# Kernel optimization log

Hardware: AMD Instinct MI355X
Metric: run time of the kernel (lower is better)

The kernel has to match this reference:

```python
import jax, jax.numpy as jnp
import numpy as np

# dims: S spaces, B batch, T tokens, D = dense_dim = concept_dim, K codebook size
S, B, T, D, K = 8, 8, 2048, 64, 512
BN_EPS = 1e-3  # keras BatchNormalization default


def setup_inputs() -> dict:
    key = jax.random.key(0)
    k0, k1, k2 = jax.random.split(key, 3)
    x = jax.random.normal(k0, (B, T, D), jnp.float32)
    W = jax.random.normal(k1, (S, D, D), jnp.float32) * 0.1   # per-space Dense kernels
    b = jnp.zeros((S, D), jnp.float32)                         # per-space Dense biases
    gamma = jnp.ones((S, D), jnp.float32)                      # BN scale
    beta = jnp.zeros((S, D), jnp.float32)                      # BN shift
    bn_mean = jnp.zeros((S, D), jnp.float32)                   # BN moving mean
    bn_var = jnp.ones((S, D), jnp.float32)                     # BN moving var
    E = jax.random.normal(k2, (S, K, D), jnp.float32)          # per-space codebooks
    return dict(x=x, W=W, b=b, gamma=gamma, beta=beta,
                bn_mean=bn_mean, bn_var=bn_var, E=E)


def reference(x, W, b, gamma, beta, bn_mean, bn_var, E):
    # per-space projection: Dense -> BatchNorm (inference) -> softmax gate
    proj = jnp.einsum('btd,sde->sbte', x, W) + b[:, None, None, :]          # [S,B,T,D]
    inv = jax.lax.rsqrt(bn_var + BN_EPS)
    bn = gamma[:, None, None, :] * (proj - bn_mean[:, None, None, :]) * inv[:, None, None, :] \
         + beta[:, None, None, :]
    att = jax.nn.softmax(bn, axis=-1)
    z = x[None] * att                                                       # z_e_att, [S,B,T,D]

    # squared euclidean distance to each code; argmin(norm) == argmin(dist^2)
    d2 = (jnp.sum(z * z, axis=-1, keepdims=True)
          - 2.0 * jnp.einsum('sbtc,skc->sbtk', z, E)
          + jnp.sum(E * E, axis=-1)[:, None, None, :])                      # [S,B,T,K]
    z_k = jnp.argmin(d2, axis=-1)                                           # [S,B,T] int

    # gather nearest codes per space, then add_n over spaces (set_att != 0)
    z_q_s = E[jnp.arange(S)[:, None, None], z_k]                            # [S,B,T,D]
    z_q = jnp.sum(z_q_s, axis=0)                                            # [B,T,D]
    z_e = jnp.sum(z, axis=0)                                                # [B,T,D]
    z_k = z_k.astype(jnp.int64) if z_k.dtype != jnp.int64 else z_k          # tf.argmin -> int64
    return z_q, z_e, z_k
```

## Files before the change

### kernel.cpp

```cpp
#include <hip/hip_runtime.h>
#include <cfloat>
#include <cmath>

#define SN 8
#define DN 64
#define KN 512
#define NN 16384
#define CK 64
#define REPAIR_THR 2e-3f
#define MAXFLAG 65536

#define WS_CNT 0
#define WS_SCL 16
#define WS_OFF (16 + SN*DN)
#define WS_E2  (WS_OFF + SN*DN)
#define WS_ENT (WS_E2 + SN*KN)
#define WS_WTH (WS_ENT + MAXFLAG)
#define WS_WTL (WS_WTH + SN*64*32)
#define WS_EH  (WS_WTL + SN*64*32)
#define WS_EL  (WS_EH + SN*KN*32)
#define WS_ZP  (WS_EL + SN*KN*32)
#define WS_END (WS_ZP + SN*NN*DN)

#define LDS_XH   0
#define LDS_XL   8192
#define LDS_WE   16384
#define LDS_ZH   32768
#define LDS_ZL   40960
#define LDS_TAIL 49152
#define LDS_TOTAL 50176

#define FB_LDS_R2    17408
#define FB_LDS_TAIL  33792
#define FB_LDS_TOTAL 34816

typedef __attribute__((ext_vector_type(8))) short bf16x8;
typedef __attribute__((ext_vector_type(4))) short s16x4;
typedef __attribute__((ext_vector_type(4))) float f32x4;

__device__ inline short bf_hi(float f, float& rem) {
    unsigned u = __float_as_uint(f);
    unsigned r = (u + 0x7fffu + ((u >> 16) & 1u)) & 0xffff0000u;
    rem = f - __uint_as_float(r);
    return (short)(r >> 16);
}
__device__ inline short bf_rn(float f) {
    unsigned u = __float_as_uint(f);
    return (short)((u + 0x7fffu + ((u >> 16) & 1u)) >> 16);
}
__device__ inline void cvt4(float a, float b, float c, float d, s16x4& h, s16x4& l) {
    float r0, r1, r2, r3;
    h.x = bf_hi(a, r0); h.y = bf_hi(b, r1); h.z = bf_hi(c, r2); h.w = bf_hi(d, r3);
    l.x = bf_rn(r0); l.y = bf_rn(r1); l.z = bf_rn(r2); l.w = bf_rn(r3);
}
__device__ inline float bf2f(unsigned short h) {
    return __uint_as_float(((unsigned)h) << 16);
}

__global__ void prep_kernel(const float* __restrict__ b, const float* __restrict__ gamma,
                            const float* __restrict__ beta, const float* __restrict__ bmean,
                            const float* __restrict__ bvar, const float* __restrict__ E,
                            float* __restrict__ ws) {
    int tid = blockIdx.x * 256 + threadIdx.x;
    if (tid < SN * KN) {
        const float* er = E + (size_t)tid * DN;
        double a = 0.0;
        for (int d = 0; d < DN; ++d) { double v = (double)er[d]; a = fma(v, v, a); }
        ws[WS_E2 + tid] = (float)a;
    }
    int u = tid - SN * KN;
    if (u >= 0 && u < SN * DN) {
        double inv = 1.0 / sqrt((double)bvar[u] + 0.001);
        double sc  = (double)gamma[u] * inv;
        ws[WS_SCL + u] = (float)sc;
        ws[WS_OFF + u] = (float)(((double)b[u] - (double)bmean[u]) * sc + (double)beta[u]);
    }
}

__global__ void prep2_kernel(const float* __restrict__ E, float* __restrict__ ws) {
    int idx = blockIdx.x * 256 + threadIdx.x;
    int sk = idx >> 4, c4 = idx & 15;
    int k = sk & (KN - 1);
    float4 g = ((const float4*)E)[(size_t)sk * 16 + c4];
    s16x4 h4, l4;
    cvt4(g.x, g.y, g.z, g.w, h4, l4);
    size_t off = ((size_t)sk * 128 + c4 * 8) ^ ((k & 7) << 4);
    *(s16x4*)((char*)(ws + WS_EH) + off) = h4;
    *(s16x4*)((char*)(ws + WS_EL) + off) = l4;
}

__global__ void prep2w_kernel(const float* __restrict__ W, float* __restrict__ ws) {
    __shared__ float wt[64][65];
    int s = blockIdx.x;
    int tid = threadIdx.x;
    #pragma unroll
    for (int r = 0; r < 4; ++r) {
        int i = r * 256 + tid;
        float4 g = ((const float4*)W)[(size_t)s * 1024 + i];
        int d = i >> 4, c4 = i & 15;
        wt[d][c4 * 4 + 0] = g.x; wt[d][c4 * 4 + 1] = g.y;
        wt[d][c4 * 4 + 2] = g.z; wt[d][c4 * 4 + 3] = g.w;
    }
    __syncthreads();
    #pragma unroll
    for (int r = 0; r < 4; ++r) {
        int j = r * 256 + tid;
        int e = j >> 4, c4 = j & 15;
        s16x4 h4, l4;
        cvt4(wt[c4 * 4 + 0][e], wt[c4 * 4 + 1][e], wt[c4 * 4 + 2][e], wt[c4 * 4 + 3][e], h4, l4);
        size_t off = ((size_t)(s * 64 + e) * 128 + c4 * 8) ^ ((e & 7) << 4);
        *(s16x4*)((char*)(ws + WS_WTH) + off) = h4;
        *(s16x4*)((char*)(ws + WS_WTL) + off) = l4;
    }
}

__launch_bounds__(256, 3)
__global__ void main_kernel(const float* __restrict__ x, float* __restrict__ ws,
                            float* __restrict__ out, int entcap) {
    extern __shared__ char smraw[];
    float* tailf = (float*)(smraw + LDS_TAIL);
    float* e2s = tailf;
    float* scl = tailf + 64;
    float* ofl = tailf + 128;
    float* zzs = tailf + 192;

    const int tid = threadIdx.x;
    const int s  = blockIdx.y;
    const int n0 = blockIdx.x * 64;

    const int lane = tid & 63;
    const int w    = tid >> 6;
    const int cc   = lane & 15;
    const int kq   = lane >> 4;

    {
        const float4* xg4 = (const float4*)x;
        #pragma unroll
        for (int r = 0; r < 4; ++r) {
            int i = r * 256 + tid;
            float4 g = xg4[n0 * 16 + i];
            int row = i >> 4, c4 = i & 15;
            s16x4 h4, l4;
            cvt4(g.x, g.y, g.z, g.w, h4, l4);
            int off = (row * 128 + c4 * 8) ^ ((row & 7) << 4);
            *(s16x4*)(smraw + LDS_XH + off) = h4;
            *(s16x4*)(smraw + LDS_XL + off) = l4;
        }
        const float4* wth4 = (const float4*)((const char*)(ws + WS_WTH) + (size_t)s * 8192);
        const float4* wtl4 = (const float4*)((const char*)(ws + WS_WTL) + (size_t)s * 8192);
        #pragma unroll
        for (int r = 0; r < 2; ++r) {
            int i = r * 256 + tid;
            ((float4*)(smraw + LDS_WE))[i] = wth4[i];
            ((float4*)(smraw + LDS_WE + 8192))[i] = wtl4[i];
        }
        if (tid < 64) { scl[tid] = ws[WS_SCL + s * 64 + tid]; ofl[tid] = ws[WS_OFF + s * 64 + tid]; }
    }
    __syncthreads();

    const int arow  = w * 16 + cc;
    const int abase = arow * 128 + kq * 16;
    const int axor  = (arow & 7) << 4;

    f32x4 pa[4];
    #pragma unroll
    for (int nt = 0; nt < 4; ++nt) pa[nt] = (f32x4){0.f, 0.f, 0.f, 0.f};
    #pragma unroll
    for (int ks = 0; ks < 2; ++ks) {
        int aoff = (abase + ks * 64) ^ axor;
        bf16x8 ah = *(const bf16x8*)(smraw + LDS_XH + aoff);
        bf16x8 al = *(const bf16x8*)(smraw + LDS_XL + aoff);
        #pragma unroll
        for (int nt = 0; nt < 4; ++nt) {
            int brow = nt * 16 + cc;
            int boff = (brow * 128 + kq * 16 + ks * 64) ^ ((brow & 7) << 4);
            bf16x8 bh = *(const bf16x8*)(smraw + LDS_WE + boff);
            bf16x8 bl = *(const bf16x8*)(smraw + LDS_WE + 8192 + boff);
            pa[nt] = __builtin_amdgcn_mfma_f32_16x16x32_bf16(ah, bh, pa[nt], 0, 0, 0);
            pa[nt] = __builtin_amdgcn_mfma_f32_16x16x32_bf16(ah, bl, pa[nt], 0, 0, 0);
            pa[nt] = __builtin_amdgcn_mfma_f32_16x16x32_bf16(al, bh, pa[nt], 0, 0, 0);
        }
    }

    {
        float sclv[4], oflv[4];
        #pragma unroll
        for (int nt = 0; nt < 4; ++nt) { sclv[nt] = scl[nt * 16 + cc]; oflv[nt] = ofl[nt * 16 + cc]; }
        #pragma unroll
        for (int r = 0; r < 4; ++r) {
            int t = w * 16 + kq * 4 + r;
            float v0 = fmaf(pa[0][r], sclv[0], oflv[0]);
            float v1 = fmaf(pa[1][r], sclv[1], oflv[1]);
            float v2 = fmaf(pa[2][r], sclv[2], oflv[2]);
            float v3 = fmaf(pa[3][r], sclv[3], oflv[3]);
            float mx = fmaxf(fmaxf(v0, v1), fmaxf(v2, v3));
            mx = fmaxf(mx, __shfl_xor(mx, 1)); mx = fmaxf(mx, __shfl_xor(mx, 2));
            mx = fmaxf(mx, __shfl_xor(mx, 4)); mx = fmaxf(mx, __shfl_xor(mx, 8));
            float e0 = expf(v0 - mx), e1 = expf(v1 - mx), e2v = expf(v2 - mx), e3 = expf(v3 - mx);
            float sm = e0 + e1 + e2v + e3;
            sm += __shfl_xor(sm, 1); sm += __shfl_xor(sm, 2);
            sm += __shfl_xor(sm, 4); sm += __shfl_xor(sm, 8);
            float inv = 1.0f / sm;
            float att[4] = { e0 * inv, e1 * inv, e2v * inv, e3 * inv };
            float zz = 0.f;
            int txor = (t & 7) << 4;
            #pragma unroll
            for (int nt = 0; nt < 4; ++nt) {
                int e = nt * 16 + cc;
                int xoff = (t * 128 + e * 2) ^ txor;
                float xv = bf2f(*(const unsigned short*)(smraw + LDS_XH + xoff))
                         + bf2f(*(const unsigned short*)(smraw + LDS_XL + xoff));
                float z = xv * att[nt];
                zz += z * z;
                float rem; short zh = bf_hi(z, rem); short zl = bf_rn(rem);
                *(short*)(smraw + LDS_ZH + xoff) = zh;
                *(short*)(smraw + LDS_ZL + xoff) = zl;
                ws[WS_ZP + ((size_t)s * NN + n0 + t) * DN + e] = z;
            }
            zz += __shfl_xor(zz, 1); zz += __shfl_xor(zz, 2);
            zz += __shfl_xor(zz, 4); zz += __shfl_xor(zz, 8);
            if (cc == 0) zzs[t] = zz;
        }
    }
    __syncthreads();

    float zzv[4];
    #pragma unroll
    for (int r = 0; r < 4; ++r) zzv[r] = zzs[w * 16 + kq * 4 + r];

    float m1[4], m2[4]; int k1[4];
    #pragma unroll
    for (int r = 0; r < 4; ++r) { m1[r] = FLT_MAX; m2[r] = FLT_MAX; k1[r] = 0x7fffffff; }

    for (int kk = 0; kk < KN; kk += CK) {
        __syncthreads();
        {
            const float4* gh4 = (const float4*)((const char*)(ws + WS_EH) + (size_t)(s * KN + kk) * 128);
            const float4* gl4 = (const float4*)((const char*)(ws + WS_EL) + (size_t)(s * KN + kk) * 128);
            #pragma unroll
            for (int r = 0; r < 2; ++r) {
                int i = r * 256 + tid;
                ((float4*)(smraw + LDS_WE))[i] = gh4[i];
                ((float4*)(smraw + LDS_WE + 8192))[i] = gl4[i];
            }
        }
        if (tid < 64) e2s[tid] = ws[WS_E2 + s * KN + kk + tid];
        __syncthreads();

        f32x4 acc[4];
        #pragma unroll
        for (int nt = 0; nt < 4; ++nt) acc[nt] = (f32x4){0.f, 0.f, 0.f, 0.f};

        #pragma unroll
        for (int ks = 0; ks < 2; ++ks) {
            int aoff = (abase + ks * 64) ^ axor;
            bf16x8 ah = *(const bf16x8*)(smraw + LDS_ZH + aoff);
            bf16x8 al = *(const bf16x8*)(smraw + LDS_ZL + aoff);
            #pragma unroll
            for (int nt = 0; nt < 4; ++nt) {
                int brow = nt * 16 + cc;
                int boff = (brow * 128 + kq * 16 + ks * 64) ^ ((brow & 7) << 4);
                bf16x8 bh = *(const bf16x8*)(smraw + LDS_WE + boff);
                bf16x8 bl = *(const bf16x8*)(smraw + LDS_WE + 8192 + boff);
                acc[nt] = __builtin_amdgcn_mfma_f32_16x16x32_bf16(ah, bh, acc[nt], 0, 0, 0);
                acc[nt] = __builtin_amdgcn_mfma_f32_16x16x32_bf16(ah, bl, acc[nt], 0, 0, 0);
                acc[nt] = __builtin_amdgcn_mfma_f32_16x16x32_bf16(al, bh, acc[nt], 0, 0, 0);
            }
        }

        #pragma unroll
        for (int nt = 0; nt < 4; ++nt) {
            float e2v = e2s[nt * 16 + cc];
            int kx = kk + nt * 16 + cc;
            #pragma unroll
            for (int r = 0; r < 4; ++r) {
                float d2 = fmaf(-2.0f, acc[nt][r], zzv[r]) + e2v;
                if (d2 < m1[r]) { m2[r] = m1[r]; m1[r] = d2; k1[r] = kx; }
                else if (d2 < m2[r]) { m2[r] = d2; }
            }
        }
    }

    #pragma unroll
    for (int mask = 1; mask <= 8; mask <<= 1) {
        #pragma unroll
        for (int r = 0; r < 4; ++r) {
            float om1 = __shfl_xor(m1[r], mask);
            int   ok1 = __shfl_xor(k1[r], mask);
            float om2 = __shfl_xor(m2[r], mask);
            bool better = (om1 < m1[r]) || (om1 == m1[r] && ok1 < k1[r]);
            float nm2 = better ? fminf(m1[r], om2) : fminf(om1, m2[r]);
            if (better) { m1[r] = om1; k1[r] = ok1; }
            m2[r] = nm2;
        }
    }
    #pragma unroll
    for (int r = 0; r < 4; ++r) {
        int n = n0 + w * 16 + kq * 4 + r;
        if (cc == 0) {
            out[2 * NN * DN + s * NN + n] = (float)k1[r];
            if (m2[r] - m1[r] < REPAIR_THR) {
                int idx = atomicAdd((int*)ws, 1);
                if (idx < entcap) ((int*)ws)[WS_ENT + idx] = (s << 14) | n;
            }
        }
    }
}

__launch_bounds__(256, 4)
__global__ void main_fb_kernel(const float* __restrict__ x, const float* __restrict__ W,
                               const float* __restrict__ E, float* __restrict__ ws,
                               float* __restrict__ out, int entcap) {
    extern __shared__ char smraw[];
    float4* xs4 = (float4*)smraw;
    float4* ws4 = (float4*)(smraw + FB_LDS_R2);
    char* ehb = smraw;
    char* elb = smraw + 8192;
    char* zhb = smraw + FB_LDS_R2;
    char* zlb = smraw + FB_LDS_R2 + 8192;
    float* tailf = (float*)(smraw + FB_LDS_TAIL);
    float* e2s = tailf; float* scl = tailf + 64; float* ofl = tailf + 128; float* zzs = tailf + 192;

    const int tid = threadIdx.x;
    const int tg = tid >> 4, lg = tid & 15;
    const int s  = blockIdx.y;
    const int n0 = blockIdx.x * 64;
    const float4* xg4 = (const float4*)x;
    const float4* Wg4 = (const float4*)W;
    const float4* Eg4 = (const float4*)E;

    #pragma unroll
    for (int r = 0; r < 4; ++r) {
        int i = r * 256 + tid;
        xs4[(i >> 4) * 17 + (i & 15)] = xg4[n0 * 16 + i];
        ws4[i] = Wg4[s * 1024 + i];
    }
    if (tid < 64) { scl[tid] = ws[WS_SCL + s * 64 + tid]; ofl[tid] = ws[WS_OFF + s * 64 + tid]; }
    __syncthreads();

    float pa[4][4];
    #pragma unroll
    for (int ti = 0; ti < 4; ++ti)
        #pragma unroll
        for (int j = 0; j < 4; ++j) pa[ti][j] = 0.f;
    #pragma unroll 4
    for (int c = 0; c < 16; ++c) {
        float4 xv[4], wv[4];
        #pragma unroll
        for (int ti = 0; ti < 4; ++ti) xv[ti] = xs4[(tg * 4 + ti) * 17 + c];
        #pragma unroll
        for (int dd = 0; dd < 4; ++dd) wv[dd] = ws4[(c * 4 + dd) * 16 + lg];
        #pragma unroll
        for (int ti = 0; ti < 4; ++ti) {
            float a0 = pa[ti][0], a1 = pa[ti][1], a2 = pa[ti][2], a3 = pa[ti][3];
            a0 = fmaf(xv[ti].x, wv[0].x, a0); a0 = fmaf(xv[ti].y, wv[1].x, a0);
            a0 = fmaf(xv[ti].z, wv[2].x, a0); a0 = fmaf(xv[ti].w, wv[3].x, a0);
            a1 = fmaf(xv[ti].x, wv[0].y, a1); a1 = fmaf(xv[ti].y, wv[1].y, a1);
            a1 = fmaf(xv[ti].z, wv[2].y, a1); a1 = fmaf(xv[ti].w, wv[3].y, a1);
            a2 = fmaf(xv[ti].x, wv[0].z, a2); a2 = fmaf(xv[ti].y, wv[1].z, a2);
            a2 = fmaf(xv[ti].z, wv[2].z, a2); a2 = fmaf(xv[ti].w, wv[3].z, a2);
            a3 = fmaf(xv[ti].x, wv[0].w, a3); a3 = fmaf(xv[ti].y, wv[1].w, a3);
            a3 = fmaf(xv[ti].z, wv[2].w, a3); a3 = fmaf(xv[ti].w, wv[3].w, a3);
            pa[ti][0] = a0; pa[ti][1] = a1; pa[ti][2] = a2; pa[ti][3] = a3;
        }
    }
    __syncthreads();

    {
        float s0 = scl[lg * 4 + 0], s1 = scl[lg * 4 + 1], s2 = scl[lg * 4 + 2], s3 = scl[lg * 4 + 3];
        float o0 = ofl[lg * 4 + 0], o1 = ofl[lg * 4 + 1], o2 = ofl[lg * 4 + 2], o3 = ofl[lg * 4 + 3];
        #pragma unroll
        for (int ti = 0; ti < 4; ++ti) {
            int t = tg * 4 + ti;
            float v0 = fmaf(pa[ti][0], s0, o0);
            float v1 = fmaf(pa[ti][1], s1, o1);
            float v2 = fmaf(pa[ti][2], s2, o2);
            float v3 = fmaf(pa[ti][3], s3, o3);
            float mx = fmaxf(fmaxf(v0, v1), fmaxf(v2, v3));
            mx = fmaxf(mx, __shfl_xor(mx, 1)); mx = fmaxf(mx, __shfl_xor(mx, 2));
            mx = fmaxf(mx, __shfl_xor(mx, 4)); mx = fmaxf(mx, __shfl_xor(mx, 8));
            float e0 = expf(v0 - mx), e1 = expf(v1 - mx), e2v = expf(v2 - mx), e3 = expf(v3 - mx);
            float sm = e0 + e1 + e2v + e3;
            sm += __shfl_xor(sm, 1); sm += __shfl_xor(sm, 2);
            sm += __shfl_xor(sm, 4); sm += __shfl_xor(sm, 8);
            float inv = 1.0f / sm;
            float4 xv = xs4[t * 17 + lg];
            float z0 = xv.x * (e0 * inv), z1 = xv.y * (e1 * inv);
            float z2 = xv.z * (e2v * inv), z3 = xv.w * (e3 * inv);
            float zz = z0 * z0 + z1 * z1 + z2 * z2 + z3 * z3;
            zz += __shfl_xor(zz, 1); zz += __shfl_xor(zz, 2);
            zz += __shfl_xor(zz, 4); zz += __shfl_xor(zz, 8);
            if (lg == 0) zzs[t] = zz;
            s16x4 h4, l4;
            cvt4(z0, z1, z2, z3, h4, l4);
            int zoff = (t * 128 + lg * 8) ^ ((t & 7) << 4);
            *(s16x4*)(zhb + zoff) = h4;
            *(s16x4*)(zlb + zoff) = l4;
            float* pz = out + NN * DN + (size_t)(n0 + t) * DN + lg * 4;
            atomicAdd(pz + 0, z0); atomicAdd(pz + 1, z1);
            atomicAdd(pz + 2, z2); atomicAdd(pz + 3, z3);
        }
    }
    __syncthreads();

    const int lane = tid & 63;
    const int w    = tid >> 6;
    const int arow = w * 16 + (lane & 15);
    const int kg16 = (lane >> 4) * 16;
    const int axor = (arow & 7) << 4;
    const int abase = arow * 128 + kg16;

    float zzv[4];
    #pragma unroll
    for (int r = 0; r < 4; ++r) zzv[r] = zzs[w * 16 + (lane >> 4) * 4 + r];

    float m1[4], m2[4]; int k1[4];
    #pragma unroll
    for (int r = 0; r < 4; ++r) { m1[r] = FLT_MAX; m2[r] = FLT_MAX; k1[r] = 0x7fffffff; }

    for (int kk = 0; kk < KN; kk += CK) {
        __syncthreads();
        #pragma unroll
        for (int r = 0; r < 4; ++r) {
            int i = r * 256 + tid;
            float4 g = Eg4[(s * KN + kk) * 16 + i];
            int row = i >> 4, c4 = i & 15;
            s16x4 h4, l4;
            cvt4(g.x, g.y, g.z, g.w, h4, l4);
            int off = (row * 128 + c4 * 8) ^ ((row & 7) << 4);
            *(s16x4*)(ehb + off) = h4;
            *(s16x4*)(elb + off) = l4;
        }
        if (tid < 64) e2s[tid] = ws[WS_E2 + s * KN + kk + tid];
        __syncthreads();

        f32x4 acc[4];
        #pragma unroll
        for (int nt = 0; nt < 4; ++nt) acc[nt] = (f32x4){0.f, 0.f, 0.f, 0.f};
        #pragma unroll
        for (int ks = 0; ks < 2; ++ks) {
            int aoff = (abase + ks * 64) ^ axor;
            bf16x8 ah = *(const bf16x8*)(zhb + aoff);
            bf16x8 al = *(const bf16x8*)(zlb + aoff);
            #pragma unroll
            for (int nt = 0; nt < 4; ++nt) {
                int brow = nt * 16 + (lane & 15);
                int boff = (brow * 128 + kg16 + ks * 64) ^ ((brow & 7) << 4);
                bf16x8 bh = *(const bf16x8*)(ehb + boff);
                bf16x8 bl = *(const bf16x8*)(elb + boff);
                acc[nt] = __builtin_amdgcn_mfma_f32_16x16x32_bf16(ah, bh, acc[nt], 0, 0, 0);
                acc[nt] = __builtin_amdgcn_mfma_f32_16x16x32_bf16(ah, bl, acc[nt], 0, 0, 0);
                acc[nt] = __builtin_amdgcn_mfma_f32_16x16x32_bf16(al, bh, acc[nt], 0, 0, 0);
            }
        }
        #pragma unroll
        for (int nt = 0; nt < 4; ++nt) {
            float e2v = e2s[nt * 16 + (lane & 15)];
            int kx = kk + nt * 16 + (lane & 15);
            #pragma unroll
            for (int r = 0; r < 4; ++r) {
                float d2 = fmaf(-2.0f, acc[nt][r], zzv[r]) + e2v;
                if (d2 < m1[r]) { m2[r] = m1[r]; m1[r] = d2; k1[r] = kx; }
                else if (d2 < m2[r]) { m2[r] = d2; }
            }
        }
    }

    #pragma unroll
    for (int mask = 1; mask <= 8; mask <<= 1) {
        #pragma unroll
        for (int r = 0; r < 4; ++r) {
            float om1 = __shfl_xor(m1[r], mask);
            int   ok1 = __shfl_xor(k1[r], mask);
            float om2 = __shfl_xor(m2[r], mask);
            bool better = (om1 < m1[r]) || (om1 == m1[r] && ok1 < k1[r]);
            float nm2 = better ? fminf(m1[r], om2) : fminf(om1, m2[r]);
            if (better) { m1[r] = om1; k1[r] = ok1; }
            m2[r] = nm2;
        }
    }
    #pragma unroll
    for (int r = 0; r < 4; ++r) {
        int t = w * 16 + (lane >> 4) * 4 + r;
        int n = n0 + t;
        if ((lane & 15) == 0) {
            out[2 * NN * DN + s * NN + n] = (float)k1[r];
            if (m2[r] - m1[r] < REPAIR_THR) {
                int idx = atomicAdd((int*)ws, 1);
                if (idx < entcap) ((int*)ws)[WS_ENT + idx] = (s << 14) | n;
            }
        }
        int kb = __shfl(k1[r], lane & 48);
        float4 eg = Eg4[(s * KN + kb) * 16 + (lane & 15)];
        float* q = out + (size_t)n * DN + (lane & 15) * 4;
        atomicAdd(q + 0, eg.x); atomicAdd(q + 1, eg.y);
        atomicAdd(q + 2, eg.z); atomicAdd(q + 3, eg.w);
    }
}

__global__ void reduce_kernel(const float* __restrict__ E, const float* __restrict__ ws,
                              float* __restrict__ out) {
    int idx = blockIdx.x * 256 + threadIdx.x;
    int n = idx >> 4, c = idx & 15;
    const float4* zp4 = (const float4*)(ws + WS_ZP);
    float4 ze = make_float4(0.f, 0.f, 0.f, 0.f);
    #pragma unroll
    for (int s = 0; s < SN; ++s) {
        float4 v = zp4[((size_t)s * NN + n) * 16 + c];
        ze.x += v.x; ze.y += v.y; ze.z += v.z; ze.w += v.w;
    }
    ((float4*)out)[NN * 16 + (size_t)n * 16 + c] = ze;

    float4 zq = make_float4(0.f, 0.f, 0.f, 0.f);
    #pragma unroll
    for (int s = 0; s < SN; ++s) {
        int k = (int)(out[2 * NN * DN + s * NN + n] + 0.5f);
        float4 e = ((const float4*)E)[((size_t)s * KN + k) * 16 + c];
        zq.x += e.x; zq.y += e.y; zq.z += e.z; zq.w += e.w;
    }
    ((float4*)out)[(size_t)n * 16 + c] = zq;
}

__global__ void repair_kernel(const float* __restrict__ x, const float* __restrict__ W,
                              const float* __restrict__ b, const float* __restrict__ gamma,
                              const float* __restrict__ beta, const float* __restrict__ bmean,
                              const float* __restrict__ bvar, const float* __restrict__ E,
                              float* __restrict__ ws, float* __restrict__ out, int entcap) {
    __shared__ double zd[64];
    __shared__ double red[256];
    __shared__ int redk[256];
    __shared__ double zzsh;
    __shared__ int shk[2];
    int cnt = ((int*)ws)[0]; if (cnt > entcap) cnt = entcap;
    const int tid = threadIdx.x;
    for (int idx = blockIdx.x; idx < cnt; idx += gridDim.x) {
        int code = ((int*)ws)[WS_ENT + idx];
        int s = code >> 14, n = code & (NN - 1);
        int e = tid & 63, q = tid >> 6;
        double p = 0.0;
        for (int d = q * 16; d < q * 16 + 16; ++d)
            p = fma((double)x[n * 64 + d], (double)W[((size_t)s * 64 + d) * 64 + e], p);
        red[tid] = p;
        __syncthreads();
        if (tid < 64) {
            double proj = (red[tid] + red[tid + 64]) + (red[tid + 128] + red[tid + 192]);
            double inv = 1.0 / sqrt((double)bvar[s * 64 + e] + 0.001);
            double bn = (double)gamma[s * 64 + e] * ((proj + (double)b[s * 64 + e]) - (double)bmean[s * 64 + e]) * inv
                      + (double)beta[s * 64 + e];
            double m = bn;
            #pragma unroll
            for (int mask = 1; mask <= 32; mask <<= 1) m = fmax(m, __shfl_xor(m, mask));
            double ex = exp(bn - m);
            double sm = ex;
            #pragma unroll
            for (int mask = 1; mask <= 32; mask <<= 1) sm += __shfl_xor(sm, mask);
            double z = (double)x[n * 64 + e] * (ex / sm);
            zd[e] = z;
            double zz = z * z;
            #pragma unroll
            for (int mask = 1; mask <= 32; mask <<= 1) zz += __shfl_xor(zz, mask);
            if (tid == 0) zzsh = zz;
        }
        __syncthreads();
        double bv = DBL_MAX; int bk = 1 << 30;
        for (int k = tid; k < KN; k += 256) {
            const float* er = E + ((size_t)s * KN + k) * 64;
            double dot = 0.0, e2 = 0.0;
            for (int d = 0; d < 64; ++d) { double ed = (double)er[d]; dot = fma(zd[d], ed, dot); e2 = fma(ed, ed, e2); }
            double d2 = (zzsh - 2.0 * dot) + e2;
            if (d2 < bv) { bv = d2; bk = k; }
        }
        #pragma unroll
        for (int mask = 1; mask <= 32; mask <<= 1) {
            double ov = __shfl_xor(bv, mask);
            int   ok = __shfl_xor(bk, mask);
            if (ov < bv || (ov == bv && ok < bk)) { bv = ov; bk = ok; }
        }
        if ((tid & 63) == 0) { red[tid >> 6] = bv; redk[tid >> 6] = bk; }
        __syncthreads();
        if (tid == 0) {
            double m = red[0]; int mk = redk[0];
            for (int i = 1; i < 4; ++i)
                if (red[i] < m || (red[i] == m && redk[i] < mk)) { m = red[i]; mk = redk[i]; }
            int kold = (int)(out[2 * NN * 64 + s * NN + n] + 0.5f);
            shk[0] = mk; shk[1] = kold;
            out[2 * NN * 64 + s * NN + n] = (float)mk;
        }
        __syncthreads();
        int mk = shk[0], kold = shk[1];
        if (mk != kold && tid < 64)
            atomicAdd(out + n * 64 + tid, E[((size_t)s * KN + mk) * 64 + tid] - E[((size_t)s * KN + kold) * 64 + tid]);
        __syncthreads();
    }
}

extern "C" void kernel_launch(void* const* d_in, const int* in_sizes, int n_in,
                              void* d_out, int out_size, void* d_ws, size_t ws_size,
                              hipStream_t stream) {
    const float* x     = (const float*)d_in[0];
    const float* W     = (const float*)d_in[1];
    const float* b     = (const float*)d_in[2];
    const float* gamma = (const float*)d_in[3];
    const float* beta  = (const float*)d_in[4];
    const float* bmean = (const float*)d_in[5];
    const float* bvar  = (const float*)d_in[6];
    const float* E     = (const float*)d_in[7];
    float* out = (float*)d_out;
    float* ws  = (float*)d_ws;

    bool staged = ws_size >= (size_t)WS_END * 4;

    long avail = (long)(ws_size / 4) - WS_ENT - 16;
    if (avail < 0) avail = 0;
    int entcap = (int)(avail > MAXFLAG ? MAXFLAG : avail);
    if (staged) entcap = MAXFLAG;

    hipMemsetAsync(d_ws, 0, 64, stream);
    prep_kernel<<<18, 256, 0, stream>>>(b, gamma, beta, bmean, bvar, E, ws);
    dim3 grid(256, 8);
    if (staged) {
        prep2w_kernel<<<8, 256, 0, stream>>>(W, ws);
        prep2_kernel<<<256, 256, 0, stream>>>(E, ws);
        main_kernel<<<grid, 256, LDS_TOTAL, stream>>>(x, ws, out, entcap);
        reduce_kernel<<<1024, 256, 0, stream>>>(E, ws, out);
    } else {
        hipMemsetAsync(d_out, 0, (size_t)(2 * NN * DN) * sizeof(float), stream);
        main_fb_kernel<<<grid, 256, FB_LDS_TOTAL, stream>>>(x, W, E, ws, out, entcap);
    }
    repair_kernel<<<2048, 256, 0, stream>>>(x, W, b, gamma, beta, bmean, bvar, E, ws, out, entcap);
}
```

Baseline: 184.4 us.

## Register-prefetch codebook tiles, pack distance and index keys, drop x/W LDS staging

The main kernel no longer stages x and W in LDS. It builds the bf16 hi/lo fragments of x in registers and reads the now-unswizzled W image straight from global memory. Codebook tiles are prefetched into registers one chunk ahead and written to a smaller LDS footprint, with launch bounds raised to four blocks per SM. The top-2 distance tracking becomes integer min/max on keys that pack a quantized distance with the code index, replacing the compare-and-branch logic. The repair kernel's fp64 loops get split accumulators for more ILP. The quantized gap threshold changes which rows get flagged for repair, and that relies on the distance range fitting the fixed-point clamp.

```diff
diff --git a/kernel.cpp b/kernel.cpp
--- a/kernel.cpp
+++ b/kernel.cpp
@@ -8,6 +8,7 @@
 #define NN 16384
 #define CK 64
 #define REPAIR_THR 2e-3f
+#define GAP_IK 8u
 #define MAXFLAG 65536
 
 #define WS_CNT 0
@@ -22,13 +23,11 @@
 #define WS_ZP  (WS_EL + SN*KN*32)
 #define WS_END (WS_ZP + SN*NN*DN)
 
-#define LDS_XH   0
-#define LDS_XL   8192
-#define LDS_WE   16384
-#define LDS_ZH   32768
-#define LDS_ZL   40960
-#define LDS_TAIL 49152
-#define LDS_TOTAL 50176
+#define LDS_ZH 0
+#define LDS_ZL 8192
+#define LDS_EH 16384
+#define LDS_EL 24576
+#define LDS_TOTAL 32768
 
 #define FB_LDS_R2    17408
 #define FB_LDS_TAIL  33792
@@ -53,9 +52,8 @@
     h.x = bf_hi(a, r0); h.y = bf_hi(b, r1); h.z = bf_hi(c, r2); h.w = bf_hi(d, r3);
     l.x = bf_rn(r0); l.y = bf_rn(r1); l.z = bf_rn(r2); l.w = bf_rn(r3);
 }
-__device__ inline float bf2f(unsigned short h) {
-    return __uint_as_float(((unsigned)h) << 16);
-}
+
+union U8 { bf16x8 v; s16x4 q[2]; };
 
 __global__ void prep_kernel(const float* __restrict__ b, const float* __restrict__ gamma,
                             const float* __restrict__ beta, const float* __restrict__ bmean,
@@ -108,198 +106,193 @@
         int e = j >> 4, c4 = j & 15;
         s16x4 h4, l4;
         cvt4(wt[c4 * 4 + 0][e], wt[c4 * 4 + 1][e], wt[c4 * 4 + 2][e], wt[c4 * 4 + 3][e], h4, l4);
-        size_t off = ((size_t)(s * 64 + e) * 128 + c4 * 8) ^ ((e & 7) << 4);
+        size_t off = (size_t)(s * 64 + e) * 128 + c4 * 8;
         *(s16x4*)((char*)(ws + WS_WTH) + off) = h4;
         *(s16x4*)((char*)(ws + WS_WTL) + off) = l4;
     }
 }
 
-__launch_bounds__(256, 3)
+__launch_bounds__(256, 4)
 __global__ void main_kernel(const float* __restrict__ x, float* __restrict__ ws,
                             float* __restrict__ out, int entcap) {
     extern __shared__ char smraw[];
-    float* tailf = (float*)(smraw + LDS_TAIL);
-    float* e2s = tailf;
-    float* scl = tailf + 64;
-    float* ofl = tailf + 128;
-    float* zzs = tailf + 192;
-
     const int tid = threadIdx.x;
     const int s  = blockIdx.y;
     const int n0 = blockIdx.x * 64;
-
     const int lane = tid & 63;
     const int w    = tid >> 6;
     const int cc   = lane & 15;
     const int kq   = lane >> 4;
-
-    {
-        const float4* xg4 = (const float4*)x;
-        #pragma unroll
-        for (int r = 0; r < 4; ++r) {
-            int i = r * 256 + tid;
-            float4 g = xg4[n0 * 16 + i];
-            int row = i >> 4, c4 = i & 15;
-            s16x4 h4, l4;
-            cvt4(g.x, g.y, g.z, g.w, h4, l4);
-            int off = (row * 128 + c4 * 8) ^ ((row & 7) << 4);
-            *(s16x4*)(smraw + LDS_XH + off) = h4;
-            *(s16x4*)(smraw + LDS_XL + off) = l4;
-        }
-        const float4* wth4 = (const float4*)((const char*)(ws + WS_WTH) + (size_t)s * 8192);
-        const float4* wtl4 = (const float4*)((const char*)(ws + WS_WTL) + (size_t)s * 8192);
-        #pragma unroll
-        for (int r = 0; r < 2; ++r) {
-            int i = r * 256 + tid;
-            ((float4*)(smraw + LDS_WE))[i] = wth4[i];
-            ((float4*)(smraw + LDS_WE + 8192))[i] = wtl4[i];
-        }
-        if (tid < 64) { scl[tid] = ws[WS_SCL + s * 64 + tid]; ofl[tid] = ws[WS_OFF + s * 64 + tid]; }
-    }
-    __syncthreads();
-
-    const int arow  = w * 16 + cc;
-    const int abase = arow * 128 + kq * 16;
-    const int axor  = (arow & 7) << 4;
-
+    const int arow = w * 16 + cc;
+    const int axor = (arow & 7) << 4;
+
+    const char* eimg_h = (const char*)(ws + WS_EH) + (size_t)s * KN * 128;
+    const char* eimg_l = (const char*)(ws + WS_EL) + (size_t)s * KN * 128;
+
+    float4 pf0 = *(const float4*)(eimg_h + tid * 16);
+    float4 pf1 = *(const float4*)(eimg_h + 4096 + tid * 16);
+    float4 pf2 = *(const float4*)(eimg_l + tid * 16);
+    float4 pf3 = *(const float4*)(eimg_l + 4096 + tid * 16);
+
+    U8 xah[2], xal[2];
+    #pragma unroll
+    for (int ks = 0; ks < 2; ++ks) {
+        const float* xr = x + (size_t)(n0 + arow) * DN + ks * 32 + kq * 8;
+        float4 a = *(const float4*)xr;
+        float4 b2 = *(const float4*)(xr + 4);
+        s16x4 h0, l0, h1, l1;
+        cvt4(a.x, a.y, a.z, a.w, h0, l0);
+        cvt4(b2.x, b2.y, b2.z, b2.w, h1, l1);
+        xah[ks].q[0] = h0; xah[ks].q[1] = h1;
+        xal[ks].q[0] = l0; xal[ks].q[1] = l1;
+    }
+
+    const char* wimg_h = (const char*)(ws + WS_WTH) + (size_t)s * 64 * 128;
+    const char* wimg_l = (const char*)(ws + WS_WTL) + (size_t)s * 64 * 128;
     f32x4 pa[4];
     #pragma unroll
     for (int nt = 0; nt < 4; ++nt) pa[nt] = (f32x4){0.f, 0.f, 0.f, 0.f};
     #pragma unroll
     for (int ks = 0; ks < 2; ++ks) {
-        int aoff = (abase + ks * 64) ^ axor;
-        bf16x8 ah = *(const bf16x8*)(smraw + LDS_XH + aoff);
-        bf16x8 al = *(const bf16x8*)(smraw + LDS_XL + aoff);
         #pragma unroll
         for (int nt = 0; nt < 4; ++nt) {
             int brow = nt * 16 + cc;
-            int boff = (brow * 128 + kq * 16 + ks * 64) ^ ((brow & 7) << 4);
-            bf16x8 bh = *(const bf16x8*)(smraw + LDS_WE + boff);
-            bf16x8 bl = *(const bf16x8*)(smraw + LDS_WE + 8192 + boff);
-            pa[nt] = __builtin_amdgcn_mfma_f32_16x16x32_bf16(ah, bh, pa[nt], 0, 0, 0);
-            pa[nt] = __builtin_amdgcn_mfma_f32_16x16x32_bf16(ah, bl, pa[nt], 0, 0, 0);
-            pa[nt] = __builtin_amdgcn_mfma_f32_16x16x32_bf16(al, bh, pa[nt], 0, 0, 0);
-        }
-    }
-
-    {
-        float sclv[4], oflv[4];
-        #pragma unroll
-        for (int nt = 0; nt < 4; ++nt) { sclv[nt] = scl[nt * 16 + cc]; oflv[nt] = ofl[nt * 16 + cc]; }
-        #pragma unroll
-        for (int r = 0; r < 4; ++r) {
-            int t = w * 16 + kq * 4 + r;
-            float v0 = fmaf(pa[0][r], sclv[0], oflv[0]);
-            float v1 = fmaf(pa[1][r], sclv[1], oflv[1]);
-            float v2 = fmaf(pa[2][r], sclv[2], oflv[2]);
-            float v3 = fmaf(pa[3][r], sclv[3], oflv[3]);
-            float mx = fmaxf(fmaxf(v0, v1), fmaxf(v2, v3));
-            mx = fmaxf(mx, __shfl_xor(mx, 1)); mx = fmaxf(mx, __shfl_xor(mx, 2));
-            mx = fmaxf(mx, __shfl_xor(mx, 4)); mx = fmaxf(mx, __shfl_xor(mx, 8));
-            float e0 = expf(v0 - mx), e1 = expf(v1 - mx), e2v = expf(v2 - mx), e3 = expf(v3 - mx);
-            float sm = e0 + e1 + e2v + e3;
-            sm += __shfl_xor(sm, 1); sm += __shfl_xor(sm, 2);
-            sm += __shfl_xor(sm, 4); sm += __shfl_xor(sm, 8);
-            float inv = 1.0f / sm;
-            float att[4] = { e0 * inv, e1 * inv, e2v * inv, e3 * inv };
-            float zz = 0.f;
-            int txor = (t & 7) << 4;
-            #pragma unroll
-            for (int nt = 0; nt < 4; ++nt) {
-                int e = nt * 16 + cc;
-                int xoff = (t * 128 + e * 2) ^ txor;
-                float xv = bf2f(*(const unsigned short*)(smraw + LDS_XH + xoff))
-                         + bf2f(*(const unsigned short*)(smraw + LDS_XL + xoff));
-                float z = xv * att[nt];
-                zz += z * z;
-                float rem; short zh = bf_hi(z, rem); short zl = bf_rn(rem);
-                *(short*)(smraw + LDS_ZH + xoff) = zh;
-                *(short*)(smraw + LDS_ZL + xoff) = zl;
-                ws[WS_ZP + ((size_t)s * NN + n0 + t) * DN + e] = z;
-            }
-            zz += __shfl_xor(zz, 1); zz += __shfl_xor(zz, 2);
-            zz += __shfl_xor(zz, 4); zz += __shfl_xor(zz, 8);
-            if (cc == 0) zzs[t] = zz;
-        }
-    }
+            bf16x8 bh = *(const bf16x8*)(wimg_h + brow * 128 + ks * 64 + kq * 16);
+            bf16x8 bl = *(const bf16x8*)(wimg_l + brow * 128 + ks * 64 + kq * 16);
+            pa[nt] = __builtin_amdgcn_mfma_f32_16x16x32_bf16(xah[ks].v, bh, pa[nt], 0, 0, 0);
+            pa[nt] = __builtin_amdgcn_mfma_f32_16x16x32_bf16(xah[ks].v, bl, pa[nt], 0, 0, 0);
+            pa[nt] = __builtin_amdgcn_mfma_f32_16x16x32_bf16(xal[ks].v, bh, pa[nt], 0, 0, 0);
+        }
+    }
+
+    float sclv[4], oflv[4];
+    #pragma unroll
+    for (int nt = 0; nt < 4; ++nt) {
+        sclv[nt] = ws[WS_SCL + s * 64 + nt * 16 + cc];
+        oflv[nt] = ws[WS_OFF + s * 64 + nt * 16 + cc];
+    }
+    float zzq[4];
+    #pragma unroll
+    for (int r = 0; r < 4; ++r) {
+        int t = w * 16 + kq * 4 + r;
+        float v0 = fmaf(pa[0][r], sclv[0], oflv[0]);
+        float v1 = fmaf(pa[1][r], sclv[1], oflv[1]);
+        float v2 = fmaf(pa[2][r], sclv[2], oflv[2]);
+        float v3 = fmaf(pa[3][r], sclv[3], oflv[3]);
+        float mx = fmaxf(fmaxf(v0, v1), fmaxf(v2, v3));
+        mx = fmaxf(mx, __shfl_xor(mx, 1)); mx = fmaxf(mx, __shfl_xor(mx, 2));
+        mx = fmaxf(mx, __shfl_xor(mx, 4)); mx = fmaxf(mx, __shfl_xor(mx, 8));
+        float e0 = expf(v0 - mx), e1 = expf(v1 - mx), e2v = expf(v2 - mx), e3 = expf(v3 - mx);
+        float sm = e0 + e1 + e2v + e3;
+        sm += __shfl_xor(sm, 1); sm += __shfl_xor(sm, 2);
+        sm += __shfl_xor(sm, 4); sm += __shfl_xor(sm, 8);
+        float inv = 1.0f / sm;
+        float att[4] = { e0 * inv, e1 * inv, e2v * inv, e3 * inv };
+        float zz = 0.f;
+        int txor = (t & 7) << 4;
+        #pragma unroll
+        for (int nt = 0; nt < 4; ++nt) {
+            int e = nt * 16 + cc;
+            float xv = x[(size_t)(n0 + t) * DN + e];
+            float z = xv * att[nt];
+            zz += z * z;
+            float rem; short zh = bf_hi(z, rem); short zl = bf_rn(rem);
+            int zoff = (t * 128 + e * 2) ^ txor;
+            *(short*)(smraw + LDS_ZH + zoff) = zh;
+            *(short*)(smraw + LDS_ZL + zoff) = zl;
+            ws[WS_ZP + ((size_t)s * NN + n0 + t) * DN + e] = z;
+        }
+        zz += __shfl_xor(zz, 1); zz += __shfl_xor(zz, 2);
+        zz += __shfl_xor(zz, 4); zz += __shfl_xor(zz, 8);
+        zzq[r] = (zz + 16.f) * 4096.f;
+    }
+    *(float4*)(smraw + LDS_EH + tid * 16) = pf0;
+    *(float4*)(smraw + LDS_EH + 4096 + tid * 16) = pf1;
+    *(float4*)(smraw + LDS_EL + tid * 16) = pf2;
+    *(float4*)(smraw + LDS_EL + 4096 + tid * 16) = pf3;
     __syncthreads();
 
-    float zzv[4];
-    #pragma unroll
-    for (int r = 0; r < 4; ++r) zzv[r] = zzs[w * 16 + kq * 4 + r];
-
-    float m1[4], m2[4]; int k1[4];
-    #pragma unroll
-    for (int r = 0; r < 4; ++r) { m1[r] = FLT_MAX; m2[r] = FLT_MAX; k1[r] = 0x7fffffff; }
+    unsigned m1[4], m2[4];
+    #pragma unroll
+    for (int r = 0; r < 4; ++r) { m1[r] = 0xFFFFFFFFu; m2[r] = 0xFFFFFFFFu; }
 
     for (int kk = 0; kk < KN; kk += CK) {
-        __syncthreads();
-        {
-            const float4* gh4 = (const float4*)((const char*)(ws + WS_EH) + (size_t)(s * KN + kk) * 128);
-            const float4* gl4 = (const float4*)((const char*)(ws + WS_EL) + (size_t)(s * KN + kk) * 128);
-            #pragma unroll
-            for (int r = 0; r < 2; ++r) {
-                int i = r * 256 + tid;
-                ((float4*)(smraw + LDS_WE))[i] = gh4[i];
-                ((float4*)(smraw + LDS_WE + 8192))[i] = gl4[i];
-            }
-        }
-        if (tid < 64) e2s[tid] = ws[WS_E2 + s * KN + kk + tid];
-        __syncthreads();
-
+        if (kk + CK < KN) {
+            const char* nbh = eimg_h + (size_t)(kk + CK) * 128;
+            const char* nbl = eimg_l + (size_t)(kk + CK) * 128;
+            pf0 = *(const float4*)(nbh + tid * 16);
+            pf1 = *(const float4*)(nbh + 4096 + tid * 16);
+            pf2 = *(const float4*)(nbl + tid * 16);
+            pf3 = *(const float4*)(nbl + 4096 + tid * 16);
+        }
+        float e2v[4];
+        #pragma unroll
+        for (int nt = 0; nt < 4; ++nt) e2v[nt] = ws[WS_E2 + s * KN + kk + nt * 16 + cc];
+
+        bf16x8 zah[2], zal[2];
+        #pragma unroll
+        for (int ks = 0; ks < 2; ++ks) {
+            int aoff = (arow * 128 + kq * 16 + ks * 64) ^ axor;
+            zah[ks] = *(const bf16x8*)(smraw + LDS_ZH + aoff);
+            zal[ks] = *(const bf16x8*)(smraw + LDS_ZL + aoff);
+        }
         f32x4 acc[4];
         #pragma unroll
         for (int nt = 0; nt < 4; ++nt) acc[nt] = (f32x4){0.f, 0.f, 0.f, 0.f};
-
         #pragma unroll
         for (int ks = 0; ks < 2; ++ks) {
-            int aoff = (abase + ks * 64) ^ axor;
-            bf16x8 ah = *(const bf16x8*)(smraw + LDS_ZH + aoff);
-            bf16x8 al = *(const bf16x8*)(smraw + LDS_ZL + aoff);
             #pragma unroll
             for (int nt = 0; nt < 4; ++nt) {
                 int brow = nt * 16 + cc;
                 int boff = (brow * 128 + kq * 16 + ks * 64) ^ ((brow & 7) << 4);
-                bf16x8 bh = *(const bf16x8*)(smraw + LDS_WE + boff);
-                bf16x8 bl = *(const bf16x8*)(smraw + LDS_WE + 8192 + boff);
-                acc[nt] = __builtin_amdgcn_mfma_f32_16x16x32_bf16(ah, bh, acc[nt], 0, 0, 0);
-                acc[nt] = __builtin_amdgcn_mfma_f32_16x16x32_bf16(ah, bl, acc[nt], 0, 0, 0);
-                acc[nt] = __builtin_amdgcn_mfma_f32_16x16x32_bf16(al, bh, acc[nt], 0, 0, 0);
+                bf16x8 bh = *(const bf16x8*)(smraw + LDS_EH + boff);
+                bf16x8 bl = *(const bf16x8*)(smraw + LDS_EL + boff);
+                acc[nt] = __builtin_amdgcn_mfma_f32_16x16x32_bf16(zah[ks], bh, acc[nt], 0, 0, 0);
+                acc[nt] = __builtin_amdgcn_mfma_f32_16x16x32_bf16(zah[ks], bl, acc[nt], 0, 0, 0);
+                acc[nt] = __builtin_amdgcn_mfma_f32_16x16x32_bf16(zal[ks], bh, acc[nt], 0, 0, 0);
             }
         }
-
         #pragma unroll
         for (int nt = 0; nt < 4; ++nt) {
-            float e2v = e2s[nt * 16 + cc];
-            int kx = kk + nt * 16 + cc;
+            unsigned kx = (unsigned)(kk + nt * 16 + cc);
+            float eb = fmaf(4096.f, e2v[nt], 0.f);
             #pragma unroll
             for (int r = 0; r < 4; ++r) {
-                float d2 = fmaf(-2.0f, acc[nt][r], zzv[r]) + e2v;
-                if (d2 < m1[r]) { m2[r] = m1[r]; m1[r] = d2; k1[r] = kx; }
-                else if (d2 < m2[r]) { m2[r] = d2; }
+                float cell = fmaf(-8192.f, acc[nt][r], zzq[r] + eb);
+                float dc = fminf(cell, 4194300.f);
+                unsigned key = (((unsigned)dc) << 9) | kx;
+                m2[r] = min(m2[r], max(m1[r], key));
+                m1[r] = min(m1[r], key);
             }
         }
+        if (kk + CK < KN) {
+            __syncthreads();
+            *(float4*)(smraw + LDS_EH + tid * 16) = pf0;
+            *(float4*)(smraw + LDS_EH + 4096 + tid * 16) = pf1;
+            *(float4*)(smraw + LDS_EL + tid * 16) = pf2;
+            *(float4*)(smraw + LDS_EL + 4096 + tid * 16) = pf3;
+            __syncthreads();
+        }
     }
 
     #pragma unroll
     for (int mask = 1; mask <= 8; mask <<= 1) {
         #pragma unroll
         for (int r = 0; r < 4; ++r) {
-            float om1 = __shfl_xor(m1[r], mask);
-            int   ok1 = __shfl_xor(k1[r], mask);
-            float om2 = __shfl_xor(m2[r], mask);
-            bool better = (om1 < m1[r]) || (om1 == m1[r] && ok1 < k1[r]);
-            float nm2 = better ? fminf(m1[r], om2) : fminf(om1, m2[r]);
-            if (better) { m1[r] = om1; k1[r] = ok1; }
-            m2[r] = nm2;
+            unsigned o1 = (unsigned)__shfl_xor((int)m1[r], mask);
+            unsigned o2 = (unsigned)__shfl_xor((int)m2[r], mask);
+            unsigned hi = max(m1[r], o1);
+            m1[r] = min(m1[r], o1);
+            m2[r] = min(min(m2[r], o2), hi);
         }
     }
     #pragma unroll
     for (int r = 0; r < 4; ++r) {
         int n = n0 + w * 16 + kq * 4 + r;
         if (cc == 0) {
-            out[2 * NN * DN + s * NN + n] = (float)k1[r];
-            if (m2[r] - m1[r] < REPAIR_THR) {
+            int k1 = (int)(m1[r] & 511u);
+            out[2 * NN * DN + s * NN + n] = (float)k1;
+            if ((m2[r] >> 9) - (m1[r] >> 9) <= GAP_IK) {
                 int idx = atomicAdd((int*)ws, 1);
                 if (idx < entcap) ((int*)ws)[WS_ENT + idx] = (s << 14) | n;
             }
@@ -537,10 +530,15 @@
         int code = ((int*)ws)[WS_ENT + idx];
         int s = code >> 14, n = code & (NN - 1);
         int e = tid & 63, q = tid >> 6;
-        double p = 0.0;
-        for (int d = q * 16; d < q * 16 + 16; ++d)
-            p = fma((double)x[n * 64 + d], (double)W[((size_t)s * 64 + d) * 64 + e], p);
-        red[tid] = p;
+        const float* xrow = x + (size_t)n * 64;
+        double p0 = 0.0, p1 = 0.0, p2 = 0.0, p3 = 0.0;
+        for (int d = q * 16; d < q * 16 + 16; d += 4) {
+            p0 = fma((double)xrow[d],     (double)W[((size_t)s * 64 + d) * 64 + e],     p0);
+            p1 = fma((double)xrow[d + 1], (double)W[((size_t)s * 64 + d + 1) * 64 + e], p1);
+            p2 = fma((double)xrow[d + 2], (double)W[((size_t)s * 64 + d + 2) * 64 + e], p2);
+            p3 = fma((double)xrow[d + 3], (double)W[((size_t)s * 64 + d + 3) * 64 + e], p3);
+        }
+        red[tid] = (p0 + p1) + (p2 + p3);
         __syncthreads();
         if (tid < 64) {
             double proj = (red[tid] + red[tid + 64]) + (red[tid + 128] + red[tid + 192]);
@@ -554,7 +552,7 @@
             double sm = ex;
             #pragma unroll
             for (int mask = 1; mask <= 32; mask <<= 1) sm += __shfl_xor(sm, mask);
-            double z = (double)x[n * 64 + e] * (ex / sm);
+            double z = (double)xrow[e] * (ex / sm);
             zd[e] = z;
             double zz = z * z;
             #pragma unroll
@@ -565,10 +563,20 @@
         double bv = DBL_MAX; int bk = 1 << 30;
         for (int k = tid; k < KN; k += 256) {
             const float* er = E + ((size_t)s * KN + k) * 64;
-            double dot = 0.0, e2 = 0.0;
-            for (int d = 0; d < 64; ++d) { double ed = (double)er[d]; dot = fma(zd[d], ed, dot); e2 = fma(ed, ed, e2); }
-            double d2 = (zzsh - 2.0 * dot) + e2;
-            if (d2 < bv) { bv = d2; bk = k; }
+            double d0 = 0.0, d1 = 0.0, d2a = 0.0, d3 = 0.0;
+            double f0 = 0.0, f1 = 0.0, f2 = 0.0, f3 = 0.0;
+            for (int d = 0; d < 64; d += 4) {
+                double e0 = (double)er[d], e1 = (double)er[d + 1];
+                double e2d = (double)er[d + 2], e3d = (double)er[d + 3];
+                d0 = fma(zd[d], e0, d0);     d1 = fma(zd[d + 1], e1, d1);
+                d2a = fma(zd[d + 2], e2d, d2a); d3 = fma(zd[d + 3], e3d, d3);
+                f0 = fma(e0, e0, f0); f1 = fma(e1, e1, f1);
+                f2 = fma(e2d, e2d, f2); f3 = fma(e3d, e3d, f3);
+            }
+            double dot = (d0 + d1) + (d2a + d3);
+            double e2t = (f0 + f1) + (f2 + f3);
+            double d2v = (zzsh - 2.0 * dot) + e2t;
+            if (d2v < bv) { bv = d2v; bk = k; }
         }
         #pragma unroll
         for (int mask = 1; mask <= 32; mask <<= 1) {
```

Result: faster. 158.5 us (-14.0%).
